# Optimization experiments

Hardware: AMD Instinct MI355X
Metric: run time of the kernel (lower is better)

## Reference

```python
import jax, jax.numpy as jnp
import numpy as np

N = 100000   # nodes
E = 1600000  # edges (avg degree 16)
H = 128      # hidden_channels
OUT = 64     # out_channels


def setup_inputs() -> dict:
    key = jax.random.key(0)
    ks = jax.random.split(key, 12)
    def lin(k, fan_in, fan_out):
        s = 1.0 / np.sqrt(fan_in)
        kw, kb = jax.random.split(k)
        W = jax.random.uniform(kw, (fan_in, fan_out), jnp.float32, -s, s)
        b = jax.random.uniform(kb, (fan_out,), jnp.float32, -s, s)
        return W, b
    W1, b1 = lin(ks[2], 1, H)
    W2, b2 = lin(ks[3], H, H)
    W3, b3 = lin(ks[4], H, H)
    Wo, bo = lin(ks[5], H, OUT)
    return {
        "x": jax.random.normal(ks[0], (N, 1), jnp.float32),
        "edge_index": jax.random.randint(ks[1], (2, E), 0, N, jnp.int32),
        "W1": W1, "b1": b1,
        "W2": W2, "b2": b2,
        "W3": W3, "b3": b3,
        "Wo": Wo, "bo": bo,
    }


def _gcn_conv(x, W, b, src, dst, dinv):
    # PyG GCNConv: x' = W x, then deg-normalized scatter-add over edges (+bias)
    h = x @ W                              # [N, C_out]
    norm = dinv[src] * dinv[dst]           # [E+N]
    msg = h[src] * norm[:, None]           # gather + scale  [E+N, C_out]
    out = jax.ops.segment_sum(msg, dst, num_segments=N)  # scatter-add
    return out + b


def reference(x, edge_index, W1, b1, W2, b2, W3, b3, Wo, bo):
    # add self-loops (GCNConv default add_self_loops=True)
    loop = jnp.arange(N, dtype=edge_index.dtype)
    src = jnp.concatenate([edge_index[0], loop])
    dst = jnp.concatenate([edge_index[1], loop])
    # symmetric normalization: deg over destination nodes, weight=1
    deg = jax.ops.segment_sum(jnp.ones_like(dst, jnp.float32), dst, num_segments=N)
    dinv = jnp.where(deg > 0, jax.lax.rsqrt(jnp.maximum(deg, 1.0)), 0.0)

    # layer 1: GCNConv -> dropout(eval=identity) -> relu
    h = jax.nn.relu(_gcn_conv(x, W1, b1, src, dst, dinv))
    # mid layer (num_layers=3 -> one mid block): GCNConv -> dropout -> relu
    h = jax.nn.relu(_gcn_conv(h, W2, b2, src, dst, dinv))
    # last layer: GCNConv -> dropout (no relu)
    h = _gcn_conv(h, W3, b3, src, dst, dinv)
    # linear head
    return h @ Wo + bo
```

## Files before the change

kernel.cpp:

```cpp
#include <hip/hip_runtime.h>

#define GN 100000
#define GE 1600000
#define GH 128
#define GOUT 64

#define NBUCK 98
#define BCAP 17664
#define P1B 98
#define P1E 16384

#define NPW 25
#define CAPE 480

typedef _Float16 half8v __attribute__((ext_vector_type(8)));
typedef _Float16 half4v __attribute__((ext_vector_type(4)));
typedef _Float16 half2v __attribute__((ext_vector_type(2)));
typedef float floatx4 __attribute__((ext_vector_type(4)));

__device__ __forceinline__ float dot2acc(half2v a, half2v b, float c) {
#if __has_builtin(__builtin_amdgcn_fdot2)
  return __builtin_amdgcn_fdot2(a, b, c, false);
#else
  return fmaf((float)a[0], (float)b[0], fmaf((float)a[1], (float)b[1], c));
#endif
}


__global__ __launch_bounds__(256) void k_prep(const float* __restrict__ W1, const float* __restrict__ b1,
                                              const float* __restrict__ W2, const float* __restrict__ W3,
                                              const float* __restrict__ Wo, const float* __restrict__ b3,
                                              const float* __restrict__ bo, unsigned* __restrict__ tabS,
                                              float* __restrict__ knots, _Float16* __restrict__ Wch,
                                              float* __restrict__ bch, int* __restrict__ rowStart,
                                              int* __restrict__ gCnt) {
  int tid = threadIdx.x;
  int blk = blockIdx.x;
  if (blk == 0) {
    __shared__ _Float16 sW2[GH * GH];
    __shared__ float sW1[GH], sb1[GH], th[GH];
    __shared__ int sidx[GH];
    for (int i = tid; i < GH * GH / 4; i += 256) {
      float4 v = ((const float4*)W2)[i];
      half4v h;
      h[0] = (_Float16)v.x; h[1] = (_Float16)v.y; h[2] = (_Float16)v.z; h[3] = (_Float16)v.w;
      ((half4v*)sW2)[i] = h;
    }
    if (tid < GH) {
      float w1 = W1[tid], bb = b1[tid];
      sW1[tid] = w1;
      sb1[tid] = bb;
      th[tid] = (w1 != 0.0f) ? (-bb / w1) : 3.0e38f;
    }
    __syncthreads();
    if (tid < GH) {
      float my = th[tid];
      int r = 0;
      for (int j = 0; j < GH; ++j) {
        float tj = th[j];
        r += (tj < my) || (tj == my && j < tid);
      }
      sidx[r] = tid;
      knots[r] = my;
    }
    __syncthreads();
    if (tid < GH) {
      int c = tid;
      float A = 0.f, B = 0.f;
      for (int k = 0; k < GH; ++k) {
        float w1 = sW1[k];
        float w2 = (float)sW2[k * GH + c];
        if (w1 < 0.0f) {
          A = fmaf(w1, w2, A);
          B = fmaf(sb1[k], w2, B);
        } else if (w1 == 0.0f && sb1[k] > 0.0f) {
          B = fmaf(sb1[k], w2, B);
        }
      }
      for (int b = 0; b <= GH; ++b) {
        half2v hh;
        hh[0] = (_Float16)A;
        hh[1] = (_Float16)B;
        tabS[((b * 64 + (c >> 1)) << 1) + (c & 1)] = __builtin_bit_cast(unsigned, hh);
        if (b < GH) {
          int k = sidx[b];
          float w1 = sW1[k];
          float w2 = (float)sW2[k * GH + c];
          if (w1 > 0.0f) {
            A = fmaf(w1, w2, A);
            B = fmaf(sb1[k], w2, B);
          } else if (w1 < 0.0f) {
            A = fmaf(-w1, w2, A);
            B = fmaf(-sb1[k], w2, B);
          }
        }
      }
    }
  } else if (blk <= 32) {
    int idx = (blk - 1) * 256 + tid;
    int k = idx >> 6, c = idx & 63;
    float s = 0.f;
#pragma unroll 8
    for (int j = 0; j < GH; ++j) s = fmaf(W3[k * GH + j], Wo[j * GOUT + c], s);
    Wch[idx] = (_Float16)s;
  } else {
    if (tid < GOUT) {
      float s = bo[tid];
      for (int j = 0; j < GH; ++j) s = fmaf(b3[j], Wo[j * GOUT + tid], s);
      bch[tid] = s;
    }
    if (tid >= 128 && tid < 128 + NBUCK) gCnt[tid - 128] = 0;
    if (tid == 255) rowStart[GN] = GE;
  }
}


__global__ __launch_bounds__(1024) void p1_fused(const int* __restrict__ ei, int* __restrict__ gCnt,
                                                 unsigned* __restrict__ staged) {
  __shared__ int cur[NBUCK];
  __shared__ int base[NBUCK];
  int tid = threadIdx.x, b = blockIdx.x;
  if (tid < NBUCK) cur[tid] = 0;
  __syncthreads();
  int e0 = b * P1E;
  int sv[16], dv[16];
#pragma unroll
  for (int k = 0; k < 16; ++k) {
    int e = e0 + k * 1024 + tid;
    if (e < GE) {
      sv[k] = ei[e];
      dv[k] = ei[GE + e];
    } else {
      sv[k] = 0;
      dv[k] = -1;
    }
  }
#pragma unroll
  for (int k = 0; k < 16; ++k) {
    if (dv[k] >= 0) atomicAdd(&cur[dv[k] >> 10], 1);
  }
  __syncthreads();
  if (tid < NBUCK) {
    base[tid] = atomicAdd(&gCnt[tid], cur[tid]);
    cur[tid] = 0;
  }
  __syncthreads();
#pragma unroll
  for (int k = 0; k < 16; ++k) {
    if (dv[k] >= 0) {
      int bb = dv[k] >> 10;
      int r = atomicAdd(&cur[bb], 1);
      int pos = base[bb] + r;
      if (pos < BCAP) staged[(size_t)bb * BCAP + pos] = ((unsigned)sv[k] << 10) | (unsigned)(dv[k] & 1023);
    }
  }
}


__global__ __launch_bounds__(1024) void p2a_build(const unsigned* __restrict__ staged,
                                                  const int* __restrict__ gCnt, const float* __restrict__ x,
                                                  float* __restrict__ dinv, float* __restrict__ xs,
                                                  int* __restrict__ rowStart) {
  __shared__ int cntL[1024];
  __shared__ int wsum[16];
  __shared__ int totL[NBUCK];
  __shared__ int baseSh;
  int b = blockIdx.x;
  int tid = threadIdx.x;
  if (tid < NBUCK) totL[tid] = gCnt[tid];
  cntL[tid] = 0;
  __syncthreads();
  if (tid == 0) {
    int s = 0;
    for (int j = 0; j < b; ++j) s += totL[j];
    baseSh = s;
  }
  int n = totL[b];
  if (n > BCAP) n = BCAP;
  __syncthreads();
  int base = baseSh;
  const unsigned* st = staged + (size_t)b * BCAP;
  for (int i = tid; i < n; i += 1024) atomicAdd(&cntL[st[i] & 1023], 1);
  __syncthreads();
  int v = cntL[tid];
  int lane = tid & 63, w = tid >> 6;
  int inc = v;
#pragma unroll
  for (int off = 1; off < 64; off <<= 1) {
    int u = __shfl_up(inc, off, 64);
    if (lane >= off) inc += u;
  }
  if (lane == 63) wsum[w] = inc;
  __syncthreads();
  int woff = 0;
  for (int i = 0; i < w; ++i) woff += wsum[i];
  int ex = inc - v + woff;
  int node = b * 1024 + tid;
  if (node < GN) {
    rowStart[node] = base + ex;
    float dv = rsqrtf((float)(v + 1));
    dinv[node] = dv;
    xs[node] = x[node] * dv;
  }
}


__global__ __launch_bounds__(1024) void p2b_scatter(const unsigned* __restrict__ staged,
                                                    const int* __restrict__ gCnt, const float* __restrict__ xs,
                                                    const float* __restrict__ dinv, const int* __restrict__ rowStart,
                                                    const float* __restrict__ knots, int* __restrict__ csr,
                                                    uint2* __restrict__ pqb) {
  __shared__ int curL[1024];
  __shared__ float accL[1024];
  __shared__ float kn[GH];
  int b = blockIdx.x;
  int tid = threadIdx.x;
  if (tid < GH) kn[tid] = knots[tid];
  int base = rowStart[b << 10];
  int node = (b << 10) + tid;
  curL[tid] = (node < GN) ? (rowStart[node] - base) : 0;
  accL[tid] = 0.f;
  int n = gCnt[b];
  if (n > BCAP) n = BCAP;
  __syncthreads();
  const unsigned* st = staged + (size_t)b * BCAP;
  int i = tid;
  for (; i + 3072 < n; i += 4096) {
    unsigned u0 = st[i], u1 = st[i + 1024], u2 = st[i + 2048], u3 = st[i + 3072];
    float x0 = xs[u0 >> 10], x1 = xs[u1 >> 10], x2 = xs[u2 >> 10], x3 = xs[u3 >> 10];
    int p0 = atomicAdd(&curL[u0 & 1023], 1);
    csr[base + p0] = (int)(u0 >> 10);
    atomicAdd(&accL[u0 & 1023], x0);
    int p1 = atomicAdd(&curL[u1 & 1023], 1);
    csr[base + p1] = (int)(u1 >> 10);
    atomicAdd(&accL[u1 & 1023], x1);
    int p2 = atomicAdd(&curL[u2 & 1023], 1);
    csr[base + p2] = (int)(u2 >> 10);
    atomicAdd(&accL[u2 & 1023], x2);
    int p3 = atomicAdd(&curL[u3 & 1023], 1);
    csr[base + p3] = (int)(u3 >> 10);
    atomicAdd(&accL[u3 & 1023], x3);
  }
  for (; i < n; i += 1024) {
    unsigned u = st[i];
    float xv = xs[u >> 10];
    int p = atomicAdd(&curL[u & 1023], 1);
    csr[base + p] = (int)(u >> 10);
    atomicAdd(&accL[u & 1023], xv);
  }
  __syncthreads();
  if (node < GN) {
    float q = dinv[node];
    float u = (accL[tid] + xs[node]) * q;
    int lo = 0;
#pragma unroll
    for (int s = 64; s > 0; s >>= 1)
      if (kn[lo + s - 1] < u) lo += s;
    if (lo < GH && kn[lo] < u) ++lo;
    half2v ph;
    ph[0] = (_Float16)(u * q);
    ph[1] = (_Float16)q;
    pqb[node] = make_uint2(__builtin_bit_cast(unsigned, ph), (unsigned)(lo << 9));
  }
}


__global__ __launch_bounds__(1024) void k_exp_full(const uint2* __restrict__ pqb, const int* __restrict__ csr,
                                                   const int* __restrict__ rowStart, const unsigned* __restrict__ tabS,
                                                   const float* __restrict__ dinv, const float* __restrict__ b2,
                                                   _Float16* __restrict__ h2out) {
  __shared__ __align__(16) uint2 sTab[129 * 64];
  __shared__ __align__(16) uint2 sBuf[16 * CAPE];
  int tid = threadIdx.x;
  {
    const uint4* tg = (const uint4*)tabS;
    uint4* td = (uint4*)sTab;
    for (int i = tid; i < 4128; i += 1024) td[i] = tg[i];
  }
  int lane = tid & 63, wv = tid >> 6;
  int wid = blockIdx.x * 16 + wv;
  int n0 = wid * NPW;
  int rsv = rowStart[n0 + (lane <= NPW ? lane : NPW)];
  int eBeg = __builtin_amdgcn_readlane(rsv, 0);
  int eTot = __builtin_amdgcn_readlane(rsv, NPW) - eBeg;
  int nE = eTot < CAPE ? eTot : CAPE;
  int srcv[8];
#pragma unroll
  for (int c = 0; c < 8; ++c) {
    int i = c * 64 + lane;
    srcv[c] = csr[i < nE ? eBeg + i : eBeg];
  }
  uint2 pv[8];
#pragma unroll
  for (int c = 0; c < 8; ++c) pv[c] = pqb[srcv[c]];
  uint2* bw = sBuf + wv * CAPE;
#pragma unroll
  for (int c = 0; c < 8; ++c) {
    int i = c * 64 + lane;
    if (i < nE) bw[i] = pv[c];
  }
  __syncthreads();

  const char* tbl = (const char*)sTab + lane * 8;
  const char* bwB = (const char*)bw;
  float2 bb = ((const float2*)b2)[lane];

  uint2 selfv = pqb[n0];
  float dvv = dinv[n0];
  uint2 selfN = pqb[n0 + 1];
  float dvN = dinv[n0 + 1];

  float a0 = 0.f, a1 = 0.f;
  auto proc = [&](uint2 v) {
    uint2 t = *(const uint2*)(tbl + v.y);
    half2v ph = __builtin_bit_cast(half2v, v.x);
    a0 = dot2acc(__builtin_bit_cast(half2v, t.x), ph, a0);
    a1 = dot2acc(__builtin_bit_cast(half2v, t.y), ph, a1);
  };

  int sB = 0;
  for (int d = 0; d < NPW; ++d) {
    int sE = __builtin_amdgcn_readlane(rsv, d + 1) - eBeg;
    a0 = 0.f;
    a1 = 0.f;
    float a2 = 0.f, a3 = 0.f;
    int lim = sE < nE ? sE : nE;
    int j = sB;
    for (; j + 8 <= lim; j += 8) {
      const char* p = bwB + (size_t)j * 8;
      uint2 v0 = *(const uint2*)(p);
      uint2 v1 = *(const uint2*)(p + 8);
      uint2 v2 = *(const uint2*)(p + 16);
      uint2 v3 = *(const uint2*)(p + 24);
      uint2 v4 = *(const uint2*)(p + 32);
      uint2 v5 = *(const uint2*)(p + 40);
      uint2 v6 = *(const uint2*)(p + 48);
      uint2 v7 = *(const uint2*)(p + 56);
      uint2 t0 = *(const uint2*)(tbl + v0.y);
      uint2 t1 = *(const uint2*)(tbl + v1.y);
      uint2 t2 = *(const uint2*)(tbl + v2.y);
      uint2 t3 = *(const uint2*)(tbl + v3.y);
      uint2 t4 = *(const uint2*)(tbl + v4.y);
      uint2 t5 = *(const uint2*)(tbl + v5.y);
      uint2 t6 = *(const uint2*)(tbl + v6.y);
      uint2 t7 = *(const uint2*)(tbl + v7.y);
      half2v p0 = __builtin_bit_cast(half2v, v0.x);
      half2v p1 = __builtin_bit_cast(half2v, v1.x);
      half2v p2 = __builtin_bit_cast(half2v, v2.x);
      half2v p3 = __builtin_bit_cast(half2v, v3.x);
      half2v p4 = __builtin_bit_cast(half2v, v4.x);
      half2v p5 = __builtin_bit_cast(half2v, v5.x);
      half2v p6 = __builtin_bit_cast(half2v, v6.x);
      half2v p7 = __builtin_bit_cast(half2v, v7.x);
      a0 = dot2acc(__builtin_bit_cast(half2v, t0.x), p0, a0);
      a1 = dot2acc(__builtin_bit_cast(half2v, t0.y), p0, a1);
      a2 = dot2acc(__builtin_bit_cast(half2v, t1.x), p1, a2);
      a3 = dot2acc(__builtin_bit_cast(half2v, t1.y), p1, a3);
      a0 = dot2acc(__builtin_bit_cast(half2v, t2.x), p2, a0);
      a1 = dot2acc(__builtin_bit_cast(half2v, t2.y), p2, a1);
      a2 = dot2acc(__builtin_bit_cast(half2v, t3.x), p3, a2);
      a3 = dot2acc(__builtin_bit_cast(half2v, t3.y), p3, a3);
      a0 = dot2acc(__builtin_bit_cast(half2v, t4.x), p4, a0);
      a1 = dot2acc(__builtin_bit_cast(half2v, t4.y), p4, a1);
      a2 = dot2acc(__builtin_bit_cast(half2v, t5.x), p5, a2);
      a3 = dot2acc(__builtin_bit_cast(half2v, t5.y), p5, a3);
      a0 = dot2acc(__builtin_bit_cast(half2v, t6.x), p6, a0);
      a1 = dot2acc(__builtin_bit_cast(half2v, t6.y), p6, a1);
      a2 = dot2acc(__builtin_bit_cast(half2v, t7.x), p7, a2);
      a3 = dot2acc(__builtin_bit_cast(half2v, t7.y), p7, a3);
    }
    for (; j + 4 <= lim; j += 4) {
      const char* p = bwB + (size_t)j * 8;
      uint2 v0 = *(const uint2*)(p);
      uint2 v1 = *(const uint2*)(p + 8);
      uint2 v2 = *(const uint2*)(p + 16);
      uint2 v3 = *(const uint2*)(p + 24);
      uint2 t0 = *(const uint2*)(tbl + v0.y);
      uint2 t1 = *(const uint2*)(tbl + v1.y);
      uint2 t2 = *(const uint2*)(tbl + v2.y);
      uint2 t3 = *(const uint2*)(tbl + v3.y);
      half2v p0 = __builtin_bit_cast(half2v, v0.x);
      half2v p1 = __builtin_bit_cast(half2v, v1.x);
      half2v p2 = __builtin_bit_cast(half2v, v2.x);
      half2v p3 = __builtin_bit_cast(half2v, v3.x);
      a0 = dot2acc(__builtin_bit_cast(half2v, t0.x), p0, a0);
      a1 = dot2acc(__builtin_bit_cast(half2v, t0.y), p0, a1);
      a2 = dot2acc(__builtin_bit_cast(half2v, t1.x), p1, a2);
      a3 = dot2acc(__builtin_bit_cast(half2v, t1.y), p1, a3);
      a0 = dot2acc(__builtin_bit_cast(half2v, t2.x), p2, a0);
      a1 = dot2acc(__builtin_bit_cast(half2v, t2.y), p2, a1);
      a2 = dot2acc(__builtin_bit_cast(half2v, t3.x), p3, a2);
      a3 = dot2acc(__builtin_bit_cast(half2v, t3.y), p3, a3);
    }
    a0 += a2;
    a1 += a3;
    for (; j < lim; ++j) proc(*(const uint2*)(bwB + (size_t)j * 8));
    for (int j2 = (sB > nE ? sB : nE); j2 < sE; ++j2) {
      int s2 = csr[eBeg + j2];
      proc(pqb[s2]);
    }
    proc(selfv);
    float r0 = fmaxf(fmaf(a0, dvv, bb.x), 0.f);
    float r1 = fmaxf(fmaf(a1, dvv, bb.y), 0.f);
    half2v o;
    o[0] = (_Float16)r0;
    o[1] = (_Float16)r1;
    ((unsigned*)h2out)[(size_t)(n0 + d) * 64 + lane] = __builtin_bit_cast(unsigned, o);
    selfv = selfN;
    dvv = dvN;
    if (d + 2 < NPW) {
      selfN = pqb[n0 + d + 2];
      dvN = dinv[n0 + d + 2];
    }
    sB = sE;
  }
}


template <int NCOL>
__global__ __launch_bounds__(256) void gemm_f16k(const _Float16* __restrict__ A, const _Float16* __restrict__ Wh,
                                                 const float* __restrict__ dinv, _Float16* __restrict__ Cout,
                                                 int ntiles) {
  constexpr int NT = NCOL / 16;
  constexpr int WS = 136;
  __shared__ __align__(16) _Float16 WtL[NCOL * WS];
  int tid = threadIdx.x;
  for (int i = tid; i < GH * NCOL; i += 256) {
    int k = i / NCOL, n = i % NCOL;
    WtL[n * WS + k] = Wh[i];
  }
  __syncthreads();
  int lane = tid & 63;
  int waveId = tid >> 6;
  int m = lane & 15, q = lane >> 4;

  for (int t = blockIdx.x * 4 + waveId; t < ntiles; t += gridDim.x * 4) {
    int row = t * 16 + m;
    const _Float16* arow = A + (size_t)row * GH + q * 8;
    half8v af[4];
#pragma unroll
    for (int ks = 0; ks < 4; ++ks) af[ks] = *(const half8v*)(arow + ks * 32);
    floatx4 acc[NT];
#pragma unroll
    for (int nt = 0; nt < NT; ++nt) {
      floatx4 z = {0.0f, 0.0f, 0.0f, 0.0f};
      acc[nt] = z;
    }
#pragma unroll
    for (int ks = 0; ks < 4; ++ks) {
#pragma unroll
      for (int nt = 0; nt < NT; ++nt) {
        half8v wf = *(const half8v*)(&WtL[(nt * 16 + m) * WS + ks * 32 + q * 8]);
        acc[nt] = __builtin_amdgcn_mfma_f32_16x16x32_f16(wf, af[ks], acc[nt], 0, 0, 0);
      }
    }
    float sc = dinv[row];
    _Float16* crow = Cout + (size_t)row * NCOL;
#pragma unroll
    for (int nt = 0; nt < NT; ++nt) {
      half4v h;
#pragma unroll
      for (int j = 0; j < 4; ++j) h[j] = (_Float16)(acc[nt][j] * sc);
      *(half4v*)(crow + nt * 16 + q * 4) = h;
    }
  }
}


__global__ __launch_bounds__(256) void k_agg64(const _Float16* __restrict__ ht, const int* __restrict__ rowStart,
                                               const int* __restrict__ csr, const float* __restrict__ dinv,
                                               const float* __restrict__ bias, float* __restrict__ out) {
  int gt = blockIdx.x * 256 + threadIdx.x;
  int wave = gt >> 6;
  int lane = threadIdx.x & 63;
  int half = lane >> 5;
  int l = lane & 31;
  int d = wave * 2 + half;
  if (d >= GN) return;
  const unsigned* htu = (const unsigned*)ht;
  half2v sv = __builtin_bit_cast(half2v, htu[(size_t)d * 32 + l]);
  float a0 = (float)sv[0], a1 = (float)sv[1];
  int e = rowStart[d];
  int en = rowStart[d + 1];
  unsigned rA0, rA1, rA2, rA3, rB0, rB1, rB2, rB3;
  bool hA = (e + 4 <= en);
  if (hA) {
    int s0 = csr[e], s1 = csr[e + 1], s2 = csr[e + 2], s3 = csr[e + 3];
    rA0 = htu[(size_t)s0 * 32 + l]; rA1 = htu[(size_t)s1 * 32 + l];
    rA2 = htu[(size_t)s2 * 32 + l]; rA3 = htu[(size_t)s3 * 32 + l];
  }
  bool hB = (e + 8 <= en);
  if (hB) {
    int s0 = csr[e + 4], s1 = csr[e + 5], s2 = csr[e + 6], s3 = csr[e + 7];
    rB0 = htu[(size_t)s0 * 32 + l]; rB1 = htu[(size_t)s1 * 32 + l];
    rB2 = htu[(size_t)s2 * 32 + l]; rB3 = htu[(size_t)s3 * 32 + l];
  }
  while (hA) {
    bool hC = (e + 12 <= en);
    unsigned rC0, rC1, rC2, rC3;
    if (hC) {
      int n0 = csr[e + 8], n1 = csr[e + 9], n2 = csr[e + 10], n3 = csr[e + 11];
      rC0 = htu[(size_t)n0 * 32 + l]; rC1 = htu[(size_t)n1 * 32 + l];
      rC2 = htu[(size_t)n2 * 32 + l]; rC3 = htu[(size_t)n3 * 32 + l];
    }
    half2v v0 = __builtin_bit_cast(half2v, rA0), v1 = __builtin_bit_cast(half2v, rA1);
    half2v v2 = __builtin_bit_cast(half2v, rA2), v3 = __builtin_bit_cast(half2v, rA3);
    a0 += (float)v0[0] + (float)v1[0] + (float)v2[0] + (float)v3[0];
    a1 += (float)v0[1] + (float)v1[1] + (float)v2[1] + (float)v3[1];
    rA0 = rB0; rA1 = rB1; rA2 = rB2; rA3 = rB3;
    rB0 = rC0; rB1 = rC1; rB2 = rC2; rB3 = rC3;
    e += 4;
    hA = hB;
    hB = hC;
  }
  for (; e < en; ++e) {
    half2v v = __builtin_bit_cast(half2v, htu[(size_t)csr[e] * 32 + l]);
    a0 += (float)v[0];
    a1 += (float)v[1];
  }
  float dv = dinv[d];
  float2 bb = ((const float2*)bias)[l];
  float2 o;
  o.x = fmaf(a0, dv, bb.x);
  o.y = fmaf(a1, dv, bb.y);
  ((float2*)out)[(size_t)d * 32 + l] = o;
}


extern "C" void kernel_launch(void* const* d_in, const int* in_sizes, int n_in,
                              void* d_out, int out_size, void* d_ws, size_t ws_size,
                              hipStream_t stream) {
  const float* x  = (const float*)d_in[0];
  const int*   ei = (const int*)d_in[1];
  const float* W1 = (const float*)d_in[2];
  const float* b1 = (const float*)d_in[3];
  const float* W2 = (const float*)d_in[4];
  const float* b2 = (const float*)d_in[5];
  const float* W3 = (const float*)d_in[6];
  const float* b3 = (const float*)d_in[7];
  const float* Wo = (const float*)d_in[8];
  const float* bo = (const float*)d_in[9];
  float* out = (float*)d_out;

  char* ws = (char*)d_ws;
  size_t off = 0;
  auto alloc = [&](size_t bytes) -> char* {
    off = (off + 255) & ~(size_t)255;
    char* p = ws + off;
    off += bytes;
    return p;
  };
  float*     dinv      = (float*)alloc((size_t)GN * 4);
  float*     xs        = (float*)alloc((size_t)GN * 4);
  int*       rowStart  = (int*)alloc((size_t)(GN + 1) * 4);
  int*       gCnt      = (int*)alloc((size_t)128 * 4);
  int*       csr       = (int*)alloc((size_t)GE * 4);
  unsigned*  tabS      = (unsigned*)alloc((size_t)129 * 128 * 4);
  float*     knots     = (float*)alloc((size_t)GH * 4);
  _Float16*  Wch       = (_Float16*)alloc((size_t)GH * GOUT * 2);
  float*     bch       = (float*)alloc((size_t)GOUT * 4);
  uint2*     pqb       = (uint2*)alloc((size_t)GN * 8);
  _Float16*  bufA      = (_Float16*)alloc((size_t)GN * GH * 2);
  _Float16*  bufB      = (_Float16*)alloc((size_t)GN * GOUT * 2);
  unsigned*  staged    = (unsigned*)bufA;
  (void)ws_size; (void)in_sizes; (void)n_in; (void)out_size;

  const int NTILES = GN / 16;
  const int GEMM_GRID = 782;

  k_prep<<<34, 256, 0, stream>>>(W1, b1, W2, W3, Wo, b3, bo, tabS, knots, Wch, bch, rowStart, gCnt);

  p1_fused<<<P1B, 1024, 0, stream>>>(ei, gCnt, staged);
  p2a_build<<<NBUCK, 1024, 0, stream>>>(staged, gCnt, x, dinv, xs, rowStart);
  p2b_scatter<<<NBUCK, 1024, 0, stream>>>(staged, gCnt, xs, dinv, rowStart, knots, csr, pqb);

  k_exp_full<<<250, 1024, 0, stream>>>(pqb, csr, rowStart, tabS, dinv, b2, bufA);

  gemm_f16k<GOUT><<<GEMM_GRID, 256, 0, stream>>>(bufA, Wch, dinv, bufB, NTILES);
  k_agg64<<<(GN / 2 + 3) / 4, 256, 0, stream>>>(bufB, rowStart, csr, dinv, bch, out);
}
```

Before: 260.4 us.

## Drop LDS edge staging in layer-2 expansion; read csr/pqb directly per edge

Removes the per-wave shared-memory staging of neighbor (pq, bucket) records and instead loads csr indices and pqb entries straight from global memory inside the unrolled edge loop. Nodes per wave drop from 25 to 13 and the grid doubles to 500 blocks. Shared-memory use falls to just the table, which allows more blocks per CU and removes the front-loaded gather plus barrier. The cost is that every lane redundantly issues the same scalar-like global loads per edge, relying on cache and broadcast.

```diff
diff --git a/kernel.cpp b/kernel.cpp
--- a/kernel.cpp
+++ b/kernel.cpp
@@ -10,8 +10,7 @@
 #define P1B 98
 #define P1E 16384
 
-#define NPW 25
-#define CAPE 480
+#define NPW 13
 
 typedef _Float16 half8v __attribute__((ext_vector_type(8)));
 typedef _Float16 half4v __attribute__((ext_vector_type(4)));
@@ -265,50 +264,41 @@
 }
 
 
-__global__ __launch_bounds__(1024) void k_exp_full(const uint2* __restrict__ pqb, const int* __restrict__ csr,
-                                                   const int* __restrict__ rowStart, const unsigned* __restrict__ tabS,
-                                                   const float* __restrict__ dinv, const float* __restrict__ b2,
-                                                   _Float16* __restrict__ h2out) {
+__global__ __launch_bounds__(1024) void k_exp_lin(const uint2* __restrict__ pqb, const int* __restrict__ csr,
+                                                  const int* __restrict__ rowStart, const unsigned* __restrict__ tabS,
+                                                  const float* __restrict__ dinv, const float* __restrict__ b2,
+                                                  _Float16* __restrict__ h2out) {
   __shared__ __align__(16) uint2 sTab[129 * 64];
-  __shared__ __align__(16) uint2 sBuf[16 * CAPE];
   int tid = threadIdx.x;
   {
     const uint4* tg = (const uint4*)tabS;
     uint4* td = (uint4*)sTab;
     for (int i = tid; i < 4128; i += 1024) td[i] = tg[i];
   }
+  __syncthreads();
   int lane = tid & 63, wv = tid >> 6;
   int wid = blockIdx.x * 16 + wv;
   int n0 = wid * NPW;
-  int rsv = rowStart[n0 + (lane <= NPW ? lane : NPW)];
-  int eBeg = __builtin_amdgcn_readlane(rsv, 0);
-  int eTot = __builtin_amdgcn_readlane(rsv, NPW) - eBeg;
-  int nE = eTot < CAPE ? eTot : CAPE;
-  int srcv[8];
-#pragma unroll
-  for (int c = 0; c < 8; ++c) {
-    int i = c * 64 + lane;
-    srcv[c] = csr[i < nE ? eBeg + i : eBeg];
-  }
-  uint2 pv[8];
-#pragma unroll
-  for (int c = 0; c < 8; ++c) pv[c] = pqb[srcv[c]];
-  uint2* bw = sBuf + wv * CAPE;
-#pragma unroll
-  for (int c = 0; c < 8; ++c) {
-    int i = c * 64 + lane;
-    if (i < nE) bw[i] = pv[c];
-  }
-  __syncthreads();
+  if (n0 >= GN) return;
+  int nCnt = NPW;
+  if (n0 + nCnt > GN) nCnt = GN - n0;
+  int wl = lane <= NPW ? lane : NPW;
+  int idx = n0 + wl;
+  if (idx > GN) idx = GN;
+  int rsv = rowStart[idx];
 
   const char* tbl = (const char*)sTab + lane * 8;
-  const char* bwB = (const char*)bw;
   float2 bb = ((const float2*)b2)[lane];
 
   uint2 selfv = pqb[n0];
   float dvv = dinv[n0];
-  uint2 selfN = pqb[n0 + 1];
-  float dvN = dinv[n0 + 1];
+  uint2 selfN;
+  float dvN = 0.f;
+  selfN.x = 0u; selfN.y = 0u;
+  if (nCnt > 1) {
+    selfN = pqb[n0 + 1];
+    dvN = dinv[n0 + 1];
+  }
 
   float a0 = 0.f, a1 = 0.f;
   auto proc = [&](uint2 v) {
@@ -318,24 +308,18 @@
     a1 = dot2acc(__builtin_bit_cast(half2v, t.y), ph, a1);
   };
 
-  int sB = 0;
-  for (int d = 0; d < NPW; ++d) {
-    int sE = __builtin_amdgcn_readlane(rsv, d + 1) - eBeg;
+  int sB = __builtin_amdgcn_readlane(rsv, 0);
+  for (int d = 0; d < nCnt; ++d) {
+    int sE = __builtin_amdgcn_readlane(rsv, d + 1);
     a0 = 0.f;
     a1 = 0.f;
     float a2 = 0.f, a3 = 0.f;
-    int lim = sE < nE ? sE : nE;
     int j = sB;
-    for (; j + 8 <= lim; j += 8) {
-      const char* p = bwB + (size_t)j * 8;
-      uint2 v0 = *(const uint2*)(p);
-      uint2 v1 = *(const uint2*)(p + 8);
-      uint2 v2 = *(const uint2*)(p + 16);
-      uint2 v3 = *(const uint2*)(p + 24);
-      uint2 v4 = *(const uint2*)(p + 32);
-      uint2 v5 = *(const uint2*)(p + 40);
-      uint2 v6 = *(const uint2*)(p + 48);
-      uint2 v7 = *(const uint2*)(p + 56);
+    for (; j + 8 <= sE; j += 8) {
+      int s0 = csr[j], s1 = csr[j + 1], s2 = csr[j + 2], s3 = csr[j + 3];
+      int s4 = csr[j + 4], s5 = csr[j + 5], s6 = csr[j + 6], s7 = csr[j + 7];
+      uint2 v0 = pqb[s0], v1 = pqb[s1], v2 = pqb[s2], v3 = pqb[s3];
+      uint2 v4 = pqb[s4], v5 = pqb[s5], v6 = pqb[s6], v7 = pqb[s7];
       uint2 t0 = *(const uint2*)(tbl + v0.y);
       uint2 t1 = *(const uint2*)(tbl + v1.y);
       uint2 t2 = *(const uint2*)(tbl + v2.y);
@@ -369,12 +353,9 @@
       a2 = dot2acc(__builtin_bit_cast(half2v, t7.x), p7, a2);
       a3 = dot2acc(__builtin_bit_cast(half2v, t7.y), p7, a3);
     }
-    for (; j + 4 <= lim; j += 4) {
-      const char* p = bwB + (size_t)j * 8;
-      uint2 v0 = *(const uint2*)(p);
-      uint2 v1 = *(const uint2*)(p + 8);
-      uint2 v2 = *(const uint2*)(p + 16);
-      uint2 v3 = *(const uint2*)(p + 24);
+    for (; j + 4 <= sE; j += 4) {
+      int s0 = csr[j], s1 = csr[j + 1], s2 = csr[j + 2], s3 = csr[j + 3];
+      uint2 v0 = pqb[s0], v1 = pqb[s1], v2 = pqb[s2], v3 = pqb[s3];
       uint2 t0 = *(const uint2*)(tbl + v0.y);
       uint2 t1 = *(const uint2*)(tbl + v1.y);
       uint2 t2 = *(const uint2*)(tbl + v2.y);
@@ -394,11 +375,7 @@
     }
     a0 += a2;
     a1 += a3;
-    for (; j < lim; ++j) proc(*(const uint2*)(bwB + (size_t)j * 8));
-    for (int j2 = (sB > nE ? sB : nE); j2 < sE; ++j2) {
-      int s2 = csr[eBeg + j2];
-      proc(pqb[s2]);
-    }
+    for (; j < sE; ++j) proc(pqb[csr[j]]);
     proc(selfv);
     float r0 = fmaxf(fmaf(a0, dvv, bb.x), 0.f);
     float r1 = fmaxf(fmaf(a1, dvv, bb.y), 0.f);
@@ -408,7 +385,7 @@
     ((unsigned*)h2out)[(size_t)(n0 + d) * 64 + lane] = __builtin_bit_cast(unsigned, o);
     selfv = selfN;
     dvv = dvN;
-    if (d + 2 < NPW) {
+    if (d + 2 < nCnt) {
       selfN = pqb[n0 + d + 2];
       dvN = dinv[n0 + d + 2];
     }
@@ -574,7 +551,7 @@
   p2a_build<<<NBUCK, 1024, 0, stream>>>(staged, gCnt, x, dinv, xs, rowStart);
   p2b_scatter<<<NBUCK, 1024, 0, stream>>>(staged, gCnt, xs, dinv, rowStart, knots, csr, pqb);
 
-  k_exp_full<<<250, 1024, 0, stream>>>(pqb, csr, rowStart, tabS, dinv, b2, bufA);
+  k_exp_lin<<<500, 1024, 0, stream>>>(pqb, csr, rowStart, tabS, dinv, b2, bufA);
 
   gemm_f16k<GOUT><<<GEMM_GRID, 256, 0, stream>>>(bufA, Wch, dinv, bufB, NTILES);
   k_agg64<<<(GN / 2 + 3) / 4, 256, 0, stream>>>(bufB, rowStart, csr, dinv, bch, out);
```

New measurement: 273.5 us. +5.0%, slower.
